# Kernel optimization log

Measured on AMD Instinct MI355X. Metric: run time of the kernel, lower is better.

Reference implementation:

```python
import jax, jax.numpy as jnp
import numpy as np

NEG = -1000000.0  # mask fill value used by the torch module


def setup_inputs() -> dict:
    key = jax.random.key(0)
    kq, kk, kv, km = jax.random.split(key, 4)
    B, Q, K, D = 8, 2048, 2048, 128
    queries = jax.random.normal(kq, (B, Q, D), dtype=jnp.float32)
    keys = jax.random.normal(kk, (B, K, D), dtype=jnp.float32)
    values = jax.random.normal(kv, (B, K, D), dtype=jnp.float32)
    attntion_mask = jax.random.randint(km, (B, K), 0, 2, dtype=jnp.int32)
    return {"queries": queries, "keys": keys, "values": values,
            "attntion_mask": attntion_mask}


def reference(queries, keys, values, attntion_mask):
    d = queries.shape[-1]
    # scores: [B, Q, K]
    scores = jnp.einsum('bqd,bkd->bqk', queries, keys) / jnp.sqrt(
        jnp.asarray(d, dtype=queries.dtype))
    # 2D mask [B, K] broadcasts over the query axis (torch repeat_interleave)
    mask = attntion_mask.astype(bool)[:, None, :]  # [B, 1, K]
    scores = jnp.where(mask, scores, NEG)
    weights = jax.nn.softmax(scores, axis=-1)
    # dropout rate is 0.0 (eval mode) -> identity
    return jnp.einsum('bqk,bkv->bqv', weights, values)
```

## Files before the change

kernel.cpp:

```cpp
#include <hip/hip_runtime.h>
#include <stdint.h>

typedef __attribute__((ext_vector_type(8))) short short8;
typedef __attribute__((ext_vector_type(4))) float f32x4;

#define NB 8
#define NQ 2048
#define NK 2048
#define ND 128
#define SCALE 0.08838834764831845f
#define L2E   1.4426950408889634f
#define FMAXC 10.0f

__device__ __forceinline__ uint32_t pk_bf16(float a, float b) {
  uint32_t ua = __builtin_bit_cast(uint32_t, a);
  uint32_t ub = __builtin_bit_cast(uint32_t, b);
  ua += 0x7FFFu + ((ua >> 16) & 1u);
  ub += 0x7FFFu + ((ub >> 16) & 1u);
  return (ua >> 16) | (ub & 0xFFFF0000u);
}

__global__ __launch_bounds__(256) void prep_kernel(const float* __restrict__ v,
                                                   const float* __restrict__ kin,
                                                   ushort* __restrict__ vt,
                                                   ushort* __restrict__ kb) {
  const int t = threadIdx.x;
  const int bid = blockIdx.x;
  if (bid < 512) {
    __shared__ __align__(16) float tile[4096];
    char* sm = (char*)tile;
    const int b = bid >> 6;
    const int k0 = ((bid >> 1) & 31) << 6;
    const int d0 = (bid & 1) << 6;
#pragma unroll
    for (int i = 0; i < 4; ++i) {
      int id = i * 256 + t;
      int k = id >> 4, c = id & 15;
      uint4 val = *(const uint4*)(v + (size_t)(b * NK + k0 + k) * ND + d0 + c * 4);
      *(uint4*)(sm + k * 256 + ((c ^ (k & 15)) * 16)) = val;
    }
    __syncthreads();
#pragma unroll
    for (int i = 0; i < 2; ++i) {
      int id = i * 256 + t;
      int d = id >> 3, kc = id & 7;
      uint32_t w[4];
#pragma unroll
      for (int jj = 0; jj < 4; ++jj) {
        int kA = kc * 8 + jj * 2, kB = kA + 1;
        float fa = *(const float*)(sm + kA * 256 + (((d >> 2) ^ (kA & 15)) * 16) + (d & 3) * 4);
        float fb = *(const float*)(sm + kB * 256 + (((d >> 2) ^ (kB & 15)) * 16) + (d & 3) * 4);
        w[jj] = pk_bf16(fa, fb);
      }
      uint4 o; o.x = w[0]; o.y = w[1]; o.z = w[2]; o.w = w[3];
      *(uint4*)(vt + (size_t)(b * ND + d0 + d) * NK + k0 + kc * 8) = o;
    }
  } else {
    int idx = (bid - 512) * 2048 + t * 8;
    f32x4 a = *(const f32x4*)(kin + idx);
    f32x4 c = *(const f32x4*)(kin + idx + 4);
    uint4 u;
    u.x = pk_bf16(a[0], a[1]); u.y = pk_bf16(a[2], a[3]);
    u.z = pk_bf16(c[0], c[1]); u.w = pk_bf16(c[2], c[3]);
    *(uint4*)(kb + idx) = u;
  }
}

#define LDS_BYTES 73728
__global__ __launch_bounds__(256) void attn_kernel(const float* __restrict__ qm,
                                                   const ushort* __restrict__ kbm,
                                                   const ushort* __restrict__ vtm,
                                                   const int* __restrict__ maskm,
                                                   ushort* __restrict__ opart,
                                                   float* __restrict__ lpart) {
  __shared__ __align__(16) char sm[LDS_BYTES];
  const int bid = blockIdx.x;
  const int b   = bid >> 6;
  const int q0  = ((bid >> 1) & 31) << 6;
  const int spl = bid & 1;
  const int kb0 = spl << 10;
  const int t = threadIdx.x;
  const int lane = t & 63;
  const int wave = t >> 6;
  const int r = lane & 15;
  const int quad = lane >> 4;
  const int half = wave >> 1;
  const int qg = wave & 1;

#define LOADK(dst, i, itv) { int id = i * 256 + t; int h = id >> 9, row = (id >> 4) & 31, c = id & 15; \
    dst = *(const uint4*)(kbm + (size_t)(b * NK + kb0 + h * 512 + (itv) * 32 + row) * ND + c * 8); }
#define STORK(src, i, base) { int id = i * 256 + t; int h = id >> 9, row = (id >> 4) & 31, c = id & 15; \
    *(uint4*)((base) + h * 8192 + row * 256 + ((c ^ (row & 15)) * 16)) = src; }
#define LOADV(dst, i, itv) { int id = i * 256 + t; int h = id >> 9, row = (id >> 2) & 127, c = id & 3; \
    dst = *(const uint4*)(vtm + (size_t)(b * ND + row) * NK + kb0 + h * 512 + (itv) * 32 + c * 8); }
#define STORV(src, i, base) { int id = i * 256 + t; int h = id >> 9, row = (id >> 2) & 127, c = id & 3; \
    *(uint4*)((base) + h * 8192 + row * 64 + ((c ^ (row & 3)) * 16)) = src; }

  short8 qf[2][4];
#pragma unroll
  for (int qt = 0; qt < 2; ++qt)
#pragma unroll
    for (int ks = 0; ks < 4; ++ks) {
      const float* p = qm + (size_t)(b * NQ + q0 + qg * 32 + qt * 16 + r) * ND + ks * 32 + quad * 8;
      f32x4 a = *(const f32x4*)p;
      f32x4 c = *(const f32x4*)(p + 4);
      uint4 u;
      u.x = pk_bf16(a[0], a[1]); u.y = pk_bf16(a[2], a[3]);
      u.z = pk_bf16(c[0], c[1]); u.w = pk_bf16(c[2], c[3]);
      qf[qt][ks] = __builtin_bit_cast(short8, u);
    }

  f32x4 oacc[2][8];
#pragma unroll
  for (int qt = 0; qt < 2; ++qt)
#pragma unroll
    for (int dt = 0; dt < 8; ++dt) oacc[qt][dt] = (f32x4){0.f, 0.f, 0.f, 0.f};
  float l_[2] = {0.f, 0.f};

  char* const pbase = sm + 65536 + wave * 2048;

  {
    uint4 ka0, ka1, ka2, ka3, va0, va1, va2, va3;
    LOADK(ka0, 0, 0) LOADK(ka1, 1, 0) LOADK(ka2, 2, 0) LOADK(ka3, 3, 0)
    LOADV(va0, 0, 0) LOADV(va1, 1, 0) LOADV(va2, 2, 0) LOADV(va3, 3, 0)
    STORK(ka0, 0, sm) STORK(ka1, 1, sm) STORK(ka2, 2, sm) STORK(ka3, 3, sm)
    char* vb = sm + 32768;
    STORV(va0, 0, vb) STORV(va1, 1, vb) STORV(va2, 2, vb) STORV(va3, 3, vb)
  }
  int4 mv0 = *(const int4*)(maskm + b * NK + kb0 + half * 512 + quad * 4);
  int4 mv1 = *(const int4*)(maskm + b * NK + kb0 + half * 512 + 16 + quad * 4);

  for (int it = 0; it < 16; ++it) {
    const int cur = it & 1;
    char* const kcur = sm + cur * 16384;
    char* const vcur = sm + 32768 + cur * 16384;
    char* const knxt = sm + (cur ^ 1) * 16384;
    char* const vnxt = sm + 32768 + (cur ^ 1) * 16384;

    __syncthreads();

    const int itn = (it < 15) ? it + 1 : 15;
    uint4 ka0, ka1, ka2, ka3, va0, va1, va2, va3;
    LOADK(ka0, 0, itn) LOADK(ka1, 1, itn) LOADK(ka2, 2, itn) LOADK(ka3, 3, itn)
    LOADV(va0, 0, itn) LOADV(va1, 1, itn) LOADV(va2, 2, itn) LOADV(va3, 3, itn)
    int4 m0n = *(const int4*)(maskm + b * NK + kb0 + half * 512 + itn * 32 + quad * 4);
    int4 m1n = *(const int4*)(maskm + b * NK + kb0 + half * 512 + itn * 32 + 16 + quad * 4);

    short8 kf[2][4];
#pragma unroll
    for (int mt = 0; mt < 2; ++mt)
#pragma unroll
      for (int ks = 0; ks < 4; ++ks)
        kf[mt][ks] = *(const short8*)(kcur + half * 8192 + (mt * 16 + r) * 256 + (((ks * 4 + quad) ^ r) * 16));
    f32x4 st[2][2];
#pragma unroll
    for (int mt = 0; mt < 2; ++mt)
#pragma unroll
      for (int qt = 0; qt < 2; ++qt) {
        f32x4 acc = (f32x4){0.f, 0.f, 0.f, 0.f};
#pragma unroll
        for (int ks = 0; ks < 4; ++ks)
          acc = __builtin_amdgcn_mfma_f32_16x16x32_bf16(kf[mt][ks], qf[qt][ks], acc, 0, 0, 0);
        st[mt][qt] = acc;
      }

    const float C1 = SCALE * L2E;
    const float C2 = -FMAXC * L2E;
#pragma unroll
    for (int qt = 0; qt < 2; ++qt) {
      float p[2][4]; float ps = 0.f;
#pragma unroll
      for (int mt = 0; mt < 2; ++mt) {
        const int4 mv = mt ? mv1 : mv0;
        float t0 = mv.x ? fmaf(st[mt][qt][0], C1, C2) : -2.0e6f;
        float t1 = mv.y ? fmaf(st[mt][qt][1], C1, C2) : -2.0e6f;
        float t2 = mv.z ? fmaf(st[mt][qt][2], C1, C2) : -2.0e6f;
        float t3 = mv.w ? fmaf(st[mt][qt][3], C1, C2) : -2.0e6f;
        p[mt][0] = exp2f(t0); p[mt][1] = exp2f(t1);
        p[mt][2] = exp2f(t2); p[mt][3] = exp2f(t3);
        ps += p[mt][0] + p[mt][1] + p[mt][2] + p[mt][3];
      }
      ps += __shfl_xor(ps, 16);
      ps += __shfl_xor(ps, 32);
      l_[qt] += ps;
#pragma unroll
      for (int mt = 0; mt < 2; ++mt) {
        uint2 w; w.x = pk_bf16(p[mt][0], p[mt][1]); w.y = pk_bf16(p[mt][2], p[mt][3]);
        *(uint2*)(pbase + (qt * 16 + r) * 64 + (((mt * 4 + quad) ^ (r & 6)) * 8)) = w;
      }
    }

    short8 pf[2];
#pragma unroll
    for (int qt = 0; qt < 2; ++qt)
      pf[qt] = *(const short8*)(pbase + (qt * 16 + r) * 64 + (((quad * 2) ^ (r & 6)) * 8));
#pragma unroll
    for (int dt = 0; dt < 8; ++dt) {
      short8 vf = *(const short8*)(vcur + half * 8192 + (dt * 16 + r) * 64 + ((quad ^ (r & 3)) * 16));
#pragma unroll
      for (int qt = 0; qt < 2; ++qt)
        oacc[qt][dt] = __builtin_amdgcn_mfma_f32_16x16x32_bf16(vf, pf[qt], oacc[qt][dt], 0, 0, 0);
    }

    STORK(ka0, 0, knxt) STORK(ka1, 1, knxt) STORK(ka2, 2, knxt) STORK(ka3, 3, knxt)
    STORV(va0, 0, vnxt) STORV(va1, 1, vnxt) STORV(va2, 2, vnxt) STORV(va3, 3, vnxt)
    mv0 = m0n; mv1 = m1n;
  }

  __syncthreads();
  float* xch = (float*)(sm + qg * 17408) + lane * 68;
  if (half == 1) {
    xch[0] = l_[0]; xch[1] = l_[1];
#pragma unroll
    for (int qt = 0; qt < 2; ++qt)
#pragma unroll
      for (int dt = 0; dt < 8; ++dt)
        *(f32x4*)(xch + 4 + (qt * 8 + dt) * 4) = oacc[qt][dt];
  }
  __syncthreads();
  if (half == 0) {
#pragma unroll
    for (int qt = 0; qt < 2; ++qt) {
      const int qrow = b * NQ + q0 + qg * 32 + qt * 16 + r;
      float lsum = l_[qt] + xch[qt];
      if (quad == 0) lpart[spl * NB * NQ + qrow] = lsum;
#pragma unroll
      for (int dt = 0; dt < 8; ++dt) {
        f32x4 o1 = *(const f32x4*)(xch + 4 + (qt * 8 + dt) * 4);
        f32x4 o = oacc[qt][dt] + o1;
        uint2 w; w.x = pk_bf16(o[0], o[1]); w.y = pk_bf16(o[2], o[3]);
        *(uint2*)(opart + (size_t)spl * NB * NQ * ND + (size_t)qrow * ND + dt * 16 + quad * 4) = w;
      }
    }
  }
}

__global__ __launch_bounds__(256) void merge_kernel(const ushort* __restrict__ opart,
                                                    const float* __restrict__ lpart,
                                                    float* __restrict__ outm) {
  const int gid = blockIdx.x * 256 + threadIdx.x;
  const int row = gid >> 4;
  const int d0 = (gid & 15) << 3;
  const size_t off = (size_t)row * ND + d0;
  uint4 u0 = *(const uint4*)(opart + off);
  uint4 u1 = *(const uint4*)(opart + (size_t)NB * NQ * ND + off);
  float inv = 1.0f / (lpart[row] + lpart[NB * NQ + row]);
  f32x4 lo, hi;
  uint32_t w;
#define UP(u, dst0, dst1) w = (u); dst0 = __builtin_bit_cast(float, w << 16); \
                          dst1 = __builtin_bit_cast(float, w & 0xFFFF0000u);
  float a0,a1,b0,b1;
  UP(u0.x, a0, a1) UP(u1.x, b0, b1) lo[0] = (a0 + b0) * inv; lo[1] = (a1 + b1) * inv;
  UP(u0.y, a0, a1) UP(u1.y, b0, b1) lo[2] = (a0 + b0) * inv; lo[3] = (a1 + b1) * inv;
  UP(u0.z, a0, a1) UP(u1.z, b0, b1) hi[0] = (a0 + b0) * inv; hi[1] = (a1 + b1) * inv;
  UP(u0.w, a0, a1) UP(u1.w, b0, b1) hi[2] = (a0 + b0) * inv; hi[3] = (a1 + b1) * inv;
#undef UP
  *(f32x4*)(outm + off) = lo;
  *(f32x4*)(outm + off + 4) = hi;
}

extern "C" void kernel_launch(void* const* d_in, const int* in_sizes, int n_in,
                              void* d_out, int out_size, void* d_ws, size_t ws_size,
                              hipStream_t stream) {
  const float* q   = (const float*)d_in[0];
  const float* k   = (const float*)d_in[1];
  const float* v   = (const float*)d_in[2];
  const int*   msk = (const int*)d_in[3];
  float* out = (float*)d_out;
  ushort* kb = (ushort*)d_ws;
  ushort* vt = kb + (size_t)NB * NK * ND;
  ushort* op = vt + (size_t)NB * NK * ND;
  float*  lp = (float*)(op + 2 * (size_t)NB * NQ * ND);

  prep_kernel<<<1536, 256, 0, stream>>>(v, k, vt, kb);
  attn_kernel<<<512, 256, 0, stream>>>(q, kb, vt, msk, op, lp);
  merge_kernel<<<1024, 256, 0, stream>>>(op, lp, out);
}
```

Baseline: 127.8 us.

## Fuse split-K merge into attention kernel and load K/V fragments directly

Each block now runs 8 waves. The four key quarters are split across wave groups inside one block, and the partials are reduced through LDS in two steps. Normalization and the fp32 output store move into the attention kernel, so the separate merge kernel and the bf16 partial buffers go away. K and V fragments are read straight from global memory into registers instead of being staged through double-buffered LDS with block-wide barriers. This trades away the partial round-trip, one launch and the per-iteration syncs, but exposes global load latency without explicit prefetch. It also duplicates K/V reads across the two query-group waves and runs with only 256 blocks.

```diff
diff --git a/kernel.cpp b/kernel.cpp
--- a/kernel.cpp
+++ b/kernel.cpp
@@ -66,35 +66,24 @@
   }
 }
 
-#define LDS_BYTES 73728
-__global__ __launch_bounds__(256) void attn_kernel(const float* __restrict__ qm,
+#define LDS_BYTES 83968
+__global__ __launch_bounds__(512) void attn_kernel(const float* __restrict__ qm,
                                                    const ushort* __restrict__ kbm,
                                                    const ushort* __restrict__ vtm,
                                                    const int* __restrict__ maskm,
-                                                   ushort* __restrict__ opart,
-                                                   float* __restrict__ lpart) {
+                                                   float* __restrict__ outm) {
   __shared__ __align__(16) char sm[LDS_BYTES];
   const int bid = blockIdx.x;
-  const int b   = bid >> 6;
-  const int q0  = ((bid >> 1) & 31) << 6;
-  const int spl = bid & 1;
-  const int kb0 = spl << 10;
+  const int b  = bid & 7;
+  const int q0 = (bid >> 3) << 6;
   const int t = threadIdx.x;
   const int lane = t & 63;
   const int wave = t >> 6;
   const int r = lane & 15;
   const int quad = lane >> 4;
+  const int qg = wave & 1;
   const int half = wave >> 1;
-  const int qg = wave & 1;
-
-#define LOADK(dst, i, itv) { int id = i * 256 + t; int h = id >> 9, row = (id >> 4) & 31, c = id & 15; \
-    dst = *(const uint4*)(kbm + (size_t)(b * NK + kb0 + h * 512 + (itv) * 32 + row) * ND + c * 8); }
-#define STORK(src, i, base) { int id = i * 256 + t; int h = id >> 9, row = (id >> 4) & 31, c = id & 15; \
-    *(uint4*)((base) + h * 8192 + row * 256 + ((c ^ (row & 15)) * 16)) = src; }
-#define LOADV(dst, i, itv) { int id = i * 256 + t; int h = id >> 9, row = (id >> 2) & 127, c = id & 3; \
-    dst = *(const uint4*)(vtm + (size_t)(b * ND + row) * NK + kb0 + h * 512 + (itv) * 32 + c * 8); }
-#define STORV(src, i, base) { int id = i * 256 + t; int h = id >> 9, row = (id >> 2) & 127, c = id & 3; \
-    *(uint4*)((base) + h * 8192 + row * 64 + ((c ^ (row & 3)) * 16)) = src; }
+  const int kh0 = half * 512;
 
   short8 qf[2][4];
 #pragma unroll
@@ -117,41 +106,26 @@
     for (int dt = 0; dt < 8; ++dt) oacc[qt][dt] = (f32x4){0.f, 0.f, 0.f, 0.f};
   float l_[2] = {0.f, 0.f};
 
-  char* const pbase = sm + 65536 + wave * 2048;
-
-  {
-    uint4 ka0, ka1, ka2, ka3, va0, va1, va2, va3;
-    LOADK(ka0, 0, 0) LOADK(ka1, 1, 0) LOADK(ka2, 2, 0) LOADK(ka3, 3, 0)
-    LOADV(va0, 0, 0) LOADV(va1, 1, 0) LOADV(va2, 2, 0) LOADV(va3, 3, 0)
-    STORK(ka0, 0, sm) STORK(ka1, 1, sm) STORK(ka2, 2, sm) STORK(ka3, 3, sm)
-    char* vb = sm + 32768;
-    STORV(va0, 0, vb) STORV(va1, 1, vb) STORV(va2, 2, vb) STORV(va3, 3, vb)
-  }
-  int4 mv0 = *(const int4*)(maskm + b * NK + kb0 + half * 512 + quad * 4);
-  int4 mv1 = *(const int4*)(maskm + b * NK + kb0 + half * 512 + 16 + quad * 4);
+  char* const pbase = sm + wave * 2048;
+  const ushort* kp = kbm + (size_t)(b * NK + kh0 + r) * ND + quad * 8;
+  const ushort* vp = vtm + (size_t)(b * ND + r) * NK + kh0 + quad * 8;
+  const int*    mp = maskm + b * NK + kh0 + quad * 4;
 
   for (int it = 0; it < 16; ++it) {
-    const int cur = it & 1;
-    char* const kcur = sm + cur * 16384;
-    char* const vcur = sm + 32768 + cur * 16384;
-    char* const knxt = sm + (cur ^ 1) * 16384;
-    char* const vnxt = sm + 32768 + (cur ^ 1) * 16384;
-
-    __syncthreads();
-
-    const int itn = (it < 15) ? it + 1 : 15;
-    uint4 ka0, ka1, ka2, ka3, va0, va1, va2, va3;
-    LOADK(ka0, 0, itn) LOADK(ka1, 1, itn) LOADK(ka2, 2, itn) LOADK(ka3, 3, itn)
-    LOADV(va0, 0, itn) LOADV(va1, 1, itn) LOADV(va2, 2, itn) LOADV(va3, 3, itn)
-    int4 m0n = *(const int4*)(maskm + b * NK + kb0 + half * 512 + itn * 32 + quad * 4);
-    int4 m1n = *(const int4*)(maskm + b * NK + kb0 + half * 512 + itn * 32 + 16 + quad * 4);
-
+    int4 mv0 = *(const int4*)(mp);
+    int4 mv1 = *(const int4*)(mp + 16);
     short8 kf[2][4];
 #pragma unroll
     for (int mt = 0; mt < 2; ++mt)
 #pragma unroll
       for (int ks = 0; ks < 4; ++ks)
-        kf[mt][ks] = *(const short8*)(kcur + half * 8192 + (mt * 16 + r) * 256 + (((ks * 4 + quad) ^ r) * 16));
+        kf[mt][ks] = *(const short8*)(kp + (size_t)mt * 16 * ND + ks * 32);
+    short8 vf[8];
+#pragma unroll
+    for (int dt = 0; dt < 8; ++dt)
+      vf[dt] = *(const short8*)(vp + (size_t)dt * 16 * NK);
+    kp += 32 * ND; vp += 32; mp += 32;
+
     f32x4 st[2][2];
 #pragma unroll
     for (int mt = 0; mt < 2; ++mt)
@@ -195,68 +169,54 @@
     for (int qt = 0; qt < 2; ++qt)
       pf[qt] = *(const short8*)(pbase + (qt * 16 + r) * 64 + (((quad * 2) ^ (r & 6)) * 8));
 #pragma unroll
-    for (int dt = 0; dt < 8; ++dt) {
-      short8 vf = *(const short8*)(vcur + half * 8192 + (dt * 16 + r) * 64 + ((quad ^ (r & 3)) * 16));
+    for (int dt = 0; dt < 8; ++dt)
 #pragma unroll
       for (int qt = 0; qt < 2; ++qt)
-        oacc[qt][dt] = __builtin_amdgcn_mfma_f32_16x16x32_bf16(vf, pf[qt], oacc[qt][dt], 0, 0, 0);
-    }
-
-    STORK(ka0, 0, knxt) STORK(ka1, 1, knxt) STORK(ka2, 2, knxt) STORK(ka3, 3, knxt)
-    STORV(va0, 0, vnxt) STORV(va1, 1, vnxt) STORV(va2, 2, vnxt) STORV(va3, 3, vnxt)
-    mv0 = m0n; mv1 = m1n;
-  }
-
-  __syncthreads();
-  float* xch = (float*)(sm + qg * 17408) + lane * 68;
-  if (half == 1) {
-    xch[0] = l_[0]; xch[1] = l_[1];
+        oacc[qt][dt] = __builtin_amdgcn_mfma_f32_16x16x32_bf16(vf[dt], pf[qt], oacc[qt][dt], 0, 0, 0);
+  }
+
+  float* slot = (float*)sm + ((size_t)(qg * 2 + (half >> 1)) * 64 + lane) * 68;
+  __syncthreads();
+  if (half & 1) {
+    slot[0] = l_[0]; slot[1] = l_[1];
 #pragma unroll
     for (int qt = 0; qt < 2; ++qt)
 #pragma unroll
       for (int dt = 0; dt < 8; ++dt)
-        *(f32x4*)(xch + 4 + (qt * 8 + dt) * 4) = oacc[qt][dt];
+        *(f32x4*)(slot + 4 + (qt * 8 + dt) * 4) = oacc[qt][dt];
+  }
+  __syncthreads();
+  if (!(half & 1)) {
+    l_[0] += slot[0]; l_[1] += slot[1];
+#pragma unroll
+    for (int qt = 0; qt < 2; ++qt)
+#pragma unroll
+      for (int dt = 0; dt < 8; ++dt)
+        oacc[qt][dt] += *(const f32x4*)(slot + 4 + (qt * 8 + dt) * 4);
+  }
+  __syncthreads();
+  float* slot2 = (float*)sm + ((size_t)(qg * 2 + 1) * 64 + lane) * 68;
+  if (half == 2) {
+    slot2[0] = l_[0]; slot2[1] = l_[1];
+#pragma unroll
+    for (int qt = 0; qt < 2; ++qt)
+#pragma unroll
+      for (int dt = 0; dt < 8; ++dt)
+        *(f32x4*)(slot2 + 4 + (qt * 8 + dt) * 4) = oacc[qt][dt];
   }
   __syncthreads();
   if (half == 0) {
 #pragma unroll
     for (int qt = 0; qt < 2; ++qt) {
-      const int qrow = b * NQ + q0 + qg * 32 + qt * 16 + r;
-      float lsum = l_[qt] + xch[qt];
-      if (quad == 0) lpart[spl * NB * NQ + qrow] = lsum;
+      float linv = 1.0f / (l_[qt] + slot2[qt]);
 #pragma unroll
       for (int dt = 0; dt < 8; ++dt) {
-        f32x4 o1 = *(const f32x4*)(xch + 4 + (qt * 8 + dt) * 4);
-        f32x4 o = oacc[qt][dt] + o1;
-        uint2 w; w.x = pk_bf16(o[0], o[1]); w.y = pk_bf16(o[2], o[3]);
-        *(uint2*)(opart + (size_t)spl * NB * NQ * ND + (size_t)qrow * ND + dt * 16 + quad * 4) = w;
-      }
-    }
-  }
-}
-
-__global__ __launch_bounds__(256) void merge_kernel(const ushort* __restrict__ opart,
-                                                    const float* __restrict__ lpart,
-                                                    float* __restrict__ outm) {
-  const int gid = blockIdx.x * 256 + threadIdx.x;
-  const int row = gid >> 4;
-  const int d0 = (gid & 15) << 3;
-  const size_t off = (size_t)row * ND + d0;
-  uint4 u0 = *(const uint4*)(opart + off);
-  uint4 u1 = *(const uint4*)(opart + (size_t)NB * NQ * ND + off);
-  float inv = 1.0f / (lpart[row] + lpart[NB * NQ + row]);
-  f32x4 lo, hi;
-  uint32_t w;
-#define UP(u, dst0, dst1) w = (u); dst0 = __builtin_bit_cast(float, w << 16); \
-                          dst1 = __builtin_bit_cast(float, w & 0xFFFF0000u);
-  float a0,a1,b0,b1;
-  UP(u0.x, a0, a1) UP(u1.x, b0, b1) lo[0] = (a0 + b0) * inv; lo[1] = (a1 + b1) * inv;
-  UP(u0.y, a0, a1) UP(u1.y, b0, b1) lo[2] = (a0 + b0) * inv; lo[3] = (a1 + b1) * inv;
-  UP(u0.z, a0, a1) UP(u1.z, b0, b1) hi[0] = (a0 + b0) * inv; hi[1] = (a1 + b1) * inv;
-  UP(u0.w, a0, a1) UP(u1.w, b0, b1) hi[2] = (a0 + b0) * inv; hi[3] = (a1 + b1) * inv;
-#undef UP
-  *(f32x4*)(outm + off) = lo;
-  *(f32x4*)(outm + off + 4) = hi;
+        f32x4 o1 = *(const f32x4*)(slot2 + 4 + (qt * 8 + dt) * 4);
+        f32x4 o = (oacc[qt][dt] + o1) * linv;
+        *(f32x4*)(outm + (size_t)(b * NQ + q0 + qg * 32 + qt * 16 + r) * ND + dt * 16 + quad * 4) = o;
+      }
+    }
+  }
 }
 
 extern "C" void kernel_launch(void* const* d_in, const int* in_sizes, int n_in,
@@ -269,10 +229,7 @@
   float* out = (float*)d_out;
   ushort* kb = (ushort*)d_ws;
   ushort* vt = kb + (size_t)NB * NK * ND;
-  ushort* op = vt + (size_t)NB * NK * ND;
-  float*  lp = (float*)(op + 2 * (size_t)NB * NQ * ND);
 
   prep_kernel<<<1536, 256, 0, stream>>>(v, k, vt, kb);
-  attn_kernel<<<512, 256, 0, stream>>>(q, kb, vt, msk, op, lp);
-  merge_kernel<<<1024, 256, 0, stream>>>(op, lp, out);
-}
+  attn_kernel<<<256, 512, 0, stream>>>(q, kb, vt, msk, out);
+}
```

Result: slower. 141.3 us (+10.6%).

## Use global_load_lds direct DMA for K/V tile prefetch into LDS

Applied to the files above, without the earlier changes.

Replaces the register-staged K and V tile loads (global load into VGPRs, then a swizzled LDS store at the end of each iteration) with global_load_lds transfers that write straight into the double-buffered LDS tiles. The XOR swizzle moves from the LDS address to the global source address. The aim is to free the staging registers and drop the ds_write instructions from the loop, so the next tile's copy overlaps the MFMA work. Mask loads are no longer prefetched and are now read at the top of each iteration. The async LDS writes depend on the compiler inserting correct vmcnt waits before the next barrier, and the mask loads now sit on the critical path.

```diff
diff --git a/kernel.cpp b/kernel.cpp
--- a/kernel.cpp
+++ b/kernel.cpp
@@ -18,6 +18,11 @@
   ua += 0x7FFFu + ((ua >> 16) & 1u);
   ub += 0x7FFFu + ((ub >> 16) & 1u);
   return (ua >> 16) | (ub & 0xFFFF0000u);
+}
+
+__device__ __forceinline__ void dma16(const void* g, void* l) {
+  __builtin_amdgcn_global_load_lds((const __attribute__((address_space(1))) void*)g,
+                                   (__attribute__((address_space(3))) void*)l, 16, 0, 0);
 }
 
 __global__ __launch_bounds__(256) void prep_kernel(const float* __restrict__ v,
@@ -87,14 +92,18 @@
   const int half = wave >> 1;
   const int qg = wave & 1;
 
-#define LOADK(dst, i, itv) { int id = i * 256 + t; int h = id >> 9, row = (id >> 4) & 31, c = id & 15; \
-    dst = *(const uint4*)(kbm + (size_t)(b * NK + kb0 + h * 512 + (itv) * 32 + row) * ND + c * 8); }
-#define STORK(src, i, base) { int id = i * 256 + t; int h = id >> 9, row = (id >> 4) & 31, c = id & 15; \
-    *(uint4*)((base) + h * 8192 + row * 256 + ((c ^ (row & 15)) * 16)) = src; }
-#define LOADV(dst, i, itv) { int id = i * 256 + t; int h = id >> 9, row = (id >> 2) & 127, c = id & 3; \
-    dst = *(const uint4*)(vtm + (size_t)(b * ND + row) * NK + kb0 + h * 512 + (itv) * 32 + c * 8); }
-#define STORV(src, i, base) { int id = i * 256 + t; int h = id >> 9, row = (id >> 2) & 127, c = id & 3; \
-    *(uint4*)((base) + h * 8192 + row * 64 + ((c ^ (row & 3)) * 16)) = src; }
+  uint32_t koff[4], voff[4];
+#pragma unroll
+  for (int j = 0; j < 4; ++j) {
+    int i = wave * 4 + j;
+    int rho = i * 4 + (lane >> 4);
+    int ck = (lane & 15) ^ (rho & 15);
+    int krow = kb0 + (rho >> 5) * 512 + (rho & 31);
+    koff[j] = (uint32_t)(b * NK + krow) * ND + ck * 8;
+    int rv = i * 16 + (lane >> 2);
+    int cv = (lane & 3) ^ (rv & 3);
+    voff[j] = (uint32_t)(b * ND + (rv & 127)) * NK + kb0 + (rv >> 7) * 512 + cv * 8;
+  }
 
   short8 qf[2][4];
 #pragma unroll
@@ -119,16 +128,11 @@
 
   char* const pbase = sm + 65536 + wave * 2048;
 
-  {
-    uint4 ka0, ka1, ka2, ka3, va0, va1, va2, va3;
-    LOADK(ka0, 0, 0) LOADK(ka1, 1, 0) LOADK(ka2, 2, 0) LOADK(ka3, 3, 0)
-    LOADV(va0, 0, 0) LOADV(va1, 1, 0) LOADV(va2, 2, 0) LOADV(va3, 3, 0)
-    STORK(ka0, 0, sm) STORK(ka1, 1, sm) STORK(ka2, 2, sm) STORK(ka3, 3, sm)
-    char* vb = sm + 32768;
-    STORV(va0, 0, vb) STORV(va1, 1, vb) STORV(va2, 2, vb) STORV(va3, 3, vb)
-  }
-  int4 mv0 = *(const int4*)(maskm + b * NK + kb0 + half * 512 + quad * 4);
-  int4 mv1 = *(const int4*)(maskm + b * NK + kb0 + half * 512 + 16 + quad * 4);
+#pragma unroll
+  for (int j = 0; j < 4; ++j) {
+    dma16(kbm + koff[j], sm + wave * 4096 + j * 1024);
+    dma16(vtm + voff[j], sm + 32768 + wave * 4096 + j * 1024);
+  }
 
   for (int it = 0; it < 16; ++it) {
     const int cur = it & 1;
@@ -139,12 +143,18 @@
 
     __syncthreads();
 
-    const int itn = (it < 15) ? it + 1 : 15;
-    uint4 ka0, ka1, ka2, ka3, va0, va1, va2, va3;
-    LOADK(ka0, 0, itn) LOADK(ka1, 1, itn) LOADK(ka2, 2, itn) LOADK(ka3, 3, itn)
-    LOADV(va0, 0, itn) LOADV(va1, 1, itn) LOADV(va2, 2, itn) LOADV(va3, 3, itn)
-    int4 m0n = *(const int4*)(maskm + b * NK + kb0 + half * 512 + itn * 32 + quad * 4);
-    int4 m1n = *(const int4*)(maskm + b * NK + kb0 + half * 512 + itn * 32 + 16 + quad * 4);
+    int4 mv0 = *(const int4*)(maskm + b * NK + kb0 + half * 512 + it * 32 + quad * 4);
+    int4 mv1 = *(const int4*)(maskm + b * NK + kb0 + half * 512 + it * 32 + 16 + quad * 4);
+
+    if (it < 15) {
+      const uint32_t kadd = (uint32_t)(it + 1) * 32 * ND;
+      const uint32_t vadd = (uint32_t)(it + 1) * 32;
+#pragma unroll
+      for (int j = 0; j < 4; ++j) {
+        dma16(kbm + koff[j] + kadd, knxt + wave * 4096 + j * 1024);
+        dma16(vtm + voff[j] + vadd, vnxt + wave * 4096 + j * 1024);
+      }
+    }
 
     short8 kf[2][4];
 #pragma unroll
@@ -201,10 +211,6 @@
       for (int qt = 0; qt < 2; ++qt)
         oacc[qt][dt] = __builtin_amdgcn_mfma_f32_16x16x32_bf16(vf, pf[qt], oacc[qt][dt], 0, 0, 0);
     }
-
-    STORK(ka0, 0, knxt) STORK(ka1, 1, knxt) STORK(ka2, 2, knxt) STORK(ka3, 3, knxt)
-    STORV(va0, 0, vnxt) STORV(va1, 1, vnxt) STORV(va2, 2, vnxt) STORV(va3, 3, vnxt)
-    mv0 = m0n; mv1 = m1n;
   }
 
   __syncthreads();
```

After: 117.7 us. -7.9%, faster.
